# Performance work log

Hardware: AMD Instinct MI355X
Metric: run time of the kernel (lower is better)

## Reference

```python
import jax, jax.numpy as jnp
import numpy as np

B, L, ENC, DEC, ATT = 256, 196, 2048, 512, 512

def setup_inputs() -> dict:
    key = jax.random.key(0)
    ks = jax.random.split(key, 8)
    s_enc = 1.0 / np.sqrt(ENC); s_dec = 1.0 / np.sqrt(DEC); s_att = 1.0 / np.sqrt(ATT)
    return {
        "encoder_out": jax.random.normal(ks[0], (B, L, ENC), dtype=jnp.float32),
        "decoder_hidden": jax.random.normal(ks[1], (B, DEC), dtype=jnp.float32),
        "W_enc": jax.random.uniform(ks[2], (ENC, ATT), jnp.float32, -s_enc, s_enc),
        "b_enc": jax.random.uniform(ks[3], (ATT,), jnp.float32, -s_enc, s_enc),
        "W_dec": jax.random.uniform(ks[4], (DEC, ATT), jnp.float32, -s_dec, s_dec),
        "b_dec": jax.random.uniform(ks[5], (ATT,), jnp.float32, -s_dec, s_dec),
        "W_att": jax.random.uniform(ks[6], (ATT, 1), jnp.float32, -s_att, s_att),
        "b_att": jax.random.uniform(ks[7], (1,), jnp.float32, -s_att, s_att),
    }

def reference(encoder_out, decoder_hidden, W_enc, b_enc, W_dec, b_dec, W_att, b_att):
    # encoder_att: [B, L, A]; decoder_att: [B, A]
    encoder_att = jnp.einsum('ble,ea->bla', encoder_out, W_enc) + b_enc
    decoder_att = decoder_hidden @ W_dec + b_dec
    hidden = jax.nn.relu(encoder_att + decoder_att[:, None, :])  # [B, L, A]
    att = jnp.einsum('bla,a->bl', hidden, W_att[:, 0]) + b_att[0]  # [B, L]
    alpha = jax.nn.softmax(att, axis=1)  # softmax over sequence dim
    awe = jnp.einsum('ble,bl->be', encoder_out, alpha)  # weighted sum
    return awe, alpha
```

## Files before the change

kernel.cpp:

```cpp
#include <hip/hip_runtime.h>
#include <hip/hip_bf16.h>
#include <stdint.h>

#define NB 256
#define NL 196
#define NE 2048
#define ND 512
#define NA 512
#define NM (NB * NL)

typedef __attribute__((ext_vector_type(4))) float f32x4;
typedef __attribute__((ext_vector_type(8))) short bf16x8;

static __device__ __forceinline__ unsigned short f2bf(float f) {
  union { float f; uint32_t u; } c; c.f = f;
  uint32_t u = c.u;
  return (unsigned short)((u + 0x7fffu + ((u >> 16) & 1u)) >> 16);
}

__global__ void k_pack_b(const float* __restrict__ W, unsigned short* __restrict__ Bp) {
  int t = blockIdx.x * 256 + threadIdx.x;
  int lane = t & 63;
  int kt32 = (t >> 6) & 63;
  int ntile = t >> 12;
  int col = ntile * 16 + (lane & 15);
  int k0 = kt32 * 32 + ((lane >> 4) << 3);
  bf16x8 o;
#pragma unroll
  for (int j = 0; j < 8; ++j) o[j] = (short)f2bf(W[(size_t)(k0 + j) * NA + col]);
  *reinterpret_cast<bf16x8*>(Bp + ((size_t)t << 3)) = o;
}

__global__ void k_dec(const float* __restrict__ dec, const float* __restrict__ Wd,
                      const float* __restrict__ bd, const float* __restrict__ be,
                      float* __restrict__ d2) {
  __shared__ float dh[ND];
  int b = blockIdx.x, tid = threadIdx.x;
  dh[tid] = dec[(size_t)b * ND + tid];
  __syncthreads();
  float s = bd[tid] + be[tid];
#pragma unroll 8
  for (int e = 0; e < ND; ++e) s = fmaf(dh[e], Wd[(size_t)e * NA + tid], s);
  d2[(size_t)b * NA + tid] = s;
}

#define BM 64
#define BK 64
#define KT (NE / BK)

__global__ __launch_bounds__(512, 4) void k_main(
    const float* __restrict__ A,
    const unsigned short* __restrict__ Bp,
    const float* __restrict__ d2,
    const float* __restrict__ Watt,
    const float* __restrict__ batt,
    float* __restrict__ att)
{
  __shared__ unsigned short As[2][BM * BK];
  __shared__ float att_w[8][BM];

  const int tid = threadIdx.x;
  const int lane = tid & 63;
  const int wid = tid >> 6;
  const int lq = lane >> 4;
  const int lr = lane & 15;
  const int row0 = blockIdx.x * BM;

  f32x4 acc[4][4];
#pragma unroll
  for (int mf = 0; mf < 4; ++mf)
#pragma unroll
    for (int r = 0; r < 4; ++r) {
      int rowg = row0 + mf * 16 + lq * 4 + r;
      int bb = rowg / NL;
      const float* d2r = d2 + (size_t)bb * NA + wid * 64 + lr;
#pragma unroll
      for (int nf = 0; nf < 4; ++nf) acc[mf][nf][r] = d2r[nf * 16];
    }

  const int srow = tid >> 3;
  const int skc = tid & 7;
  const float* ag = A + (size_t)(row0 + srow) * NE + skc * 8;
  const int swz_w = srow * 64 + ((skc ^ (srow & 7)) << 3);

  auto cvt_store = [&](int buf, const f32x4& a, const f32x4& b) {
    bf16x8 o;
    o[0] = (short)f2bf(a[0]); o[1] = (short)f2bf(a[1]);
    o[2] = (short)f2bf(a[2]); o[3] = (short)f2bf(a[3]);
    o[4] = (short)f2bf(b[0]); o[5] = (short)f2bf(b[1]);
    o[6] = (short)f2bf(b[2]); o[7] = (short)f2bf(b[3]);
    *reinterpret_cast<bf16x8*>(&As[buf][swz_w]) = o;
  };

  {
    f32x4 p0 = *reinterpret_cast<const f32x4*>(ag);
    f32x4 p1 = *reinterpret_cast<const f32x4*>(ag + 4);
    cvt_store(0, p0, p1);
  }
  __syncthreads();

  const unsigned short* bpw = Bp + (size_t)(wid * 4) * 32768 + lane * 8;

  for (int kt = 0; kt < KT; ++kt) {
    const int cur = kt & 1;
    f32x4 n0, n1;
    if (kt < KT - 1) {
      const float* agn = ag + (size_t)(kt + 1) * BK;
      n0 = *reinterpret_cast<const f32x4*>(agn);
      n1 = *reinterpret_cast<const f32x4*>(agn + 4);
    }
    bf16x8 bf[4][2];
#pragma unroll
    for (int nf = 0; nf < 4; ++nf)
#pragma unroll
      for (int ks = 0; ks < 2; ++ks)
        bf[nf][ks] = *reinterpret_cast<const bf16x8*>(bpw + (size_t)nf * 32768 + (kt * 2 + ks) * 512);
#pragma unroll
    for (int ks = 0; ks < 2; ++ks)
#pragma unroll
      for (int mf = 0; mf < 4; ++mf) {
        const int rrow = mf * 16 + lr;
        const int chunk = (ks * 4 + lq) ^ (lr & 7);
        bf16x8 af = *reinterpret_cast<const bf16x8*>(&As[cur][rrow * 64 + (chunk << 3)]);
#pragma unroll
        for (int nf = 0; nf < 4; ++nf)
          acc[mf][nf] = __builtin_amdgcn_mfma_f32_16x16x32_bf16(af, bf[nf][ks], acc[mf][nf], 0, 0, 0);
      }
    if (kt < KT - 1) cvt_store(cur ^ 1, n0, n1);
    __syncthreads();
  }

  float w[4];
#pragma unroll
  for (int nf = 0; nf < 4; ++nf) w[nf] = Watt[wid * 64 + nf * 16 + lr];
#pragma unroll
  for (int mf = 0; mf < 4; ++mf)
#pragma unroll
    for (int r = 0; r < 4; ++r) {
      float s = 0.f;
#pragma unroll
      for (int nf = 0; nf < 4; ++nf) s = fmaf(fmaxf(acc[mf][nf][r], 0.f), w[nf], s);
      s += __shfl_xor(s, 1);
      s += __shfl_xor(s, 2);
      s += __shfl_xor(s, 4);
      s += __shfl_xor(s, 8);
      if (lr == 0) att_w[wid][mf * 16 + lq * 4 + r] = s;
    }
  __syncthreads();
  if (tid < BM) {
    float s = 0.f;
#pragma unroll
    for (int wv = 0; wv < 8; ++wv) s += att_w[wv][tid];
    att[row0 + tid] = s + batt[0];
  }
}

__global__ void k_softmax(float* __restrict__ alpha) {
  int b = blockIdx.x, lane = threadIdx.x;
  float* ar = alpha + (size_t)b * NL;
  float v[4];
#pragma unroll
  for (int i = 0; i < 4; ++i) {
    int l = i * 64 + lane;
    v[i] = (l < NL) ? ar[l] : -1e30f;
  }
  float m = fmaxf(fmaxf(v[0], v[1]), fmaxf(v[2], v[3]));
#pragma unroll
  for (int o = 32; o >= 1; o >>= 1) m = fmaxf(m, __shfl_xor(m, o));
  float e[4];
  float s = 0.f;
#pragma unroll
  for (int i = 0; i < 4; ++i) {
    int l = i * 64 + lane;
    e[i] = (l < NL) ? __expf(v[i] - m) : 0.f;
    s += e[i];
  }
#pragma unroll
  for (int o = 32; o >= 1; o >>= 1) s += __shfl_xor(s, o);
  float inv = 1.f / s;
#pragma unroll
  for (int i = 0; i < 4; ++i) {
    int l = i * 64 + lane;
    if (l < NL) ar[l] = e[i] * inv;
  }
}

__global__ void k_awe(const float* __restrict__ enc, const float* __restrict__ alpha,
                      float* __restrict__ awe) {
  __shared__ float al[NL];
  int b = blockIdx.y, ch = blockIdx.x, tid = threadIdx.x;
  if (tid < NL) al[tid] = alpha[(size_t)b * NL + tid];
  __syncthreads();
  int e0 = ch * 1024 + tid * 4;
  const float* ep = enc + (size_t)b * NL * NE + e0;
  f32x4 s = {0.f, 0.f, 0.f, 0.f};
#pragma unroll 4
  for (int l = 0; l < NL; ++l) {
    f32x4 v = *reinterpret_cast<const f32x4*>(ep + (size_t)l * NE);
    float a = al[l];
    s[0] = fmaf(a, v[0], s[0]);
    s[1] = fmaf(a, v[1], s[1]);
    s[2] = fmaf(a, v[2], s[2]);
    s[3] = fmaf(a, v[3], s[3]);
  }
  *reinterpret_cast<f32x4*>(awe + (size_t)b * NE + e0) = s;
}

extern "C" void kernel_launch(void* const* d_in, const int* in_sizes, int n_in,
                              void* d_out, int out_size, void* d_ws, size_t ws_size,
                              hipStream_t stream) {
  const float* enc  = (const float*)d_in[0];
  const float* dec  = (const float*)d_in[1];
  const float* Wenc = (const float*)d_in[2];
  const float* benc = (const float*)d_in[3];
  const float* Wdec = (const float*)d_in[4];
  const float* bdec = (const float*)d_in[5];
  const float* Watt = (const float*)d_in[6];
  const float* batt = (const float*)d_in[7];

  float* awe   = (float*)d_out;
  float* alpha = (float*)d_out + (size_t)NB * NE;

  char* ws = (char*)d_ws;
  unsigned short* Bp = (unsigned short*)ws;
  float* d2 = (float*)(ws + (size_t)2 * 1024 * 1024);

  k_pack_b<<<dim3(512), dim3(256), 0, stream>>>(Wenc, Bp);
  k_dec<<<dim3(NB), dim3(512), 0, stream>>>(dec, Wdec, bdec, benc, d2);
  k_main<<<dim3(NM / BM), dim3(512), 0, stream>>>(enc, Bp, d2, Watt, batt, alpha);
  k_softmax<<<dim3(NB), dim3(64), 0, stream>>>(alpha);
  k_awe<<<dim3(2, NB), dim3(256), 0, stream>>>(enc, alpha, awe);
}
```

Before: 264.5 us.

## Merge prep kernels and fuse softmax into weighted-sum kernel

New measurement: 256.8 us. 1.03x faster.

```diff
diff --git a/kernel.cpp b/kernel.cpp
--- a/kernel.cpp
+++ b/kernel.cpp
@@ -13,35 +13,38 @@
 typedef __attribute__((ext_vector_type(8))) short bf16x8;
 
 static __device__ __forceinline__ unsigned short f2bf(float f) {
-  union { float f; uint32_t u; } c; c.f = f;
-  uint32_t u = c.u;
-  return (unsigned short)((u + 0x7fffu + ((u >> 16) & 1u)) >> 16);
-}
-
-__global__ void k_pack_b(const float* __restrict__ W, unsigned short* __restrict__ Bp) {
-  int t = blockIdx.x * 256 + threadIdx.x;
-  int lane = t & 63;
-  int kt32 = (t >> 6) & 63;
-  int ntile = t >> 12;
-  int col = ntile * 16 + (lane & 15);
-  int k0 = kt32 * 32 + ((lane >> 4) << 3);
-  bf16x8 o;
-#pragma unroll
-  for (int j = 0; j < 8; ++j) o[j] = (short)f2bf(W[(size_t)(k0 + j) * NA + col]);
-  *reinterpret_cast<bf16x8*>(Bp + ((size_t)t << 3)) = o;
-}
-
-__global__ void k_dec(const float* __restrict__ dec, const float* __restrict__ Wd,
-                      const float* __restrict__ bd, const float* __restrict__ be,
-                      float* __restrict__ d2) {
-  __shared__ float dh[ND];
-  int b = blockIdx.x, tid = threadIdx.x;
-  dh[tid] = dec[(size_t)b * ND + tid];
-  __syncthreads();
-  float s = bd[tid] + be[tid];
+  __hip_bfloat16 h = __float2bfloat16(f);
+  unsigned short u;
+  __builtin_memcpy(&u, &h, 2);
+  return u;
+}
+
+__global__ __launch_bounds__(512) void k_prep(
+    const float* __restrict__ W, unsigned short* __restrict__ Bp,
+    const float* __restrict__ dec, const float* __restrict__ Wd,
+    const float* __restrict__ bd, const float* __restrict__ be,
+    float* __restrict__ d2) {
+  if (blockIdx.x < 256) {
+    int t = blockIdx.x * 512 + threadIdx.x;
+    int lane = t & 63;
+    int kt32 = (t >> 6) & 63;
+    int ntile = t >> 12;
+    int col = ntile * 16 + (lane & 15);
+    int k0 = kt32 * 32 + ((lane >> 4) << 3);
+    bf16x8 o;
+#pragma unroll
+    for (int j = 0; j < 8; ++j) o[j] = (short)f2bf(W[(size_t)(k0 + j) * NA + col]);
+    *reinterpret_cast<bf16x8*>(Bp + ((size_t)t << 3)) = o;
+  } else {
+    __shared__ float dh[ND];
+    int b = blockIdx.x - 256, tid = threadIdx.x;
+    dh[tid] = dec[(size_t)b * ND + tid];
+    __syncthreads();
+    float s = bd[tid] + be[tid];
 #pragma unroll 8
-  for (int e = 0; e < ND; ++e) s = fmaf(dh[e], Wd[(size_t)e * NA + tid], s);
-  d2[(size_t)b * NA + tid] = s;
+    for (int e = 0; e < ND; ++e) s = fmaf(dh[e], Wd[(size_t)e * NA + tid], s);
+    d2[(size_t)b * NA + tid] = s;
+  }
 }
 
 #define BM 64
@@ -155,55 +158,68 @@
   }
 }
 
-__global__ void k_softmax(float* __restrict__ alpha) {
-  int b = blockIdx.x, lane = threadIdx.x;
-  float* ar = alpha + (size_t)b * NL;
-  float v[4];
-#pragma unroll
-  for (int i = 0; i < 4; ++i) {
-    int l = i * 64 + lane;
-    v[i] = (l < NL) ? ar[l] : -1e30f;
-  }
-  float m = fmaxf(fmaxf(v[0], v[1]), fmaxf(v[2], v[3]));
-#pragma unroll
-  for (int o = 32; o >= 1; o >>= 1) m = fmaxf(m, __shfl_xor(m, o));
-  float e[4];
-  float s = 0.f;
-#pragma unroll
-  for (int i = 0; i < 4; ++i) {
-    int l = i * 64 + lane;
-    e[i] = (l < NL) ? __expf(v[i] - m) : 0.f;
-    s += e[i];
-  }
-#pragma unroll
-  for (int o = 32; o >= 1; o >>= 1) s += __shfl_xor(s, o);
-  float inv = 1.f / s;
-#pragma unroll
-  for (int i = 0; i < 4; ++i) {
-    int l = i * 64 + lane;
-    if (l < NL) ar[l] = e[i] * inv;
-  }
-}
-
-__global__ void k_awe(const float* __restrict__ enc, const float* __restrict__ alpha,
-                      float* __restrict__ awe) {
-  __shared__ float al[NL];
-  int b = blockIdx.y, ch = blockIdx.x, tid = threadIdx.x;
-  if (tid < NL) al[tid] = alpha[(size_t)b * NL + tid];
+__global__ __launch_bounds__(512) void k_awe(
+    const float* __restrict__ enc, const float* __restrict__ att,
+    float* __restrict__ alpha_out, float* __restrict__ awe) {
+  __shared__ float al[256];
+  const int b = blockIdx.x, tid = threadIdx.x;
+
+  if (tid < 64) {
+    const int lane = tid;
+    const float* ar = att + (size_t)b * NL;
+    float v[4];
+#pragma unroll
+    for (int i = 0; i < 4; ++i) {
+      int l = i * 64 + lane;
+      v[i] = (l < NL) ? ar[l] : -1e30f;
+    }
+    float m = fmaxf(fmaxf(v[0], v[1]), fmaxf(v[2], v[3]));
+#pragma unroll
+    for (int o = 32; o >= 1; o >>= 1) m = fmaxf(m, __shfl_xor(m, o));
+    float e[4];
+    float s = 0.f;
+#pragma unroll
+    for (int i = 0; i < 4; ++i) {
+      int l = i * 64 + lane;
+      e[i] = (l < NL) ? __expf(v[i] - m) : 0.f;
+      s += e[i];
+    }
+#pragma unroll
+    for (int o = 32; o >= 1; o >>= 1) s += __shfl_xor(s, o);
+    float inv = 1.f / s;
+#pragma unroll
+    for (int i = 0; i < 4; ++i) {
+      int l = i * 64 + lane;
+      if (l < NL) {
+        float a = e[i] * inv;
+        al[l] = a;
+        alpha_out[(size_t)b * NL + l] = a;
+      }
+    }
+  }
   __syncthreads();
-  int e0 = ch * 1024 + tid * 4;
-  const float* ep = enc + (size_t)b * NL * NE + e0;
-  f32x4 s = {0.f, 0.f, 0.f, 0.f};
-#pragma unroll 4
-  for (int l = 0; l < NL; ++l) {
-    f32x4 v = *reinterpret_cast<const f32x4*>(ep + (size_t)l * NE);
-    float a = al[l];
-    s[0] = fmaf(a, v[0], s[0]);
-    s[1] = fmaf(a, v[1], s[1]);
-    s[2] = fmaf(a, v[2], s[2]);
-    s[3] = fmaf(a, v[3], s[3]);
-  }
-  *reinterpret_cast<f32x4*>(awe + (size_t)b * NE + e0) = s;
+
+  const float* ep = enc + (size_t)b * NL * NE + tid * 4;
+  f32x4 a0 = {0.f, 0.f, 0.f, 0.f}, a1 = a0, a2 = a0, a3 = a0;
+#pragma unroll 2
+  for (int l = 0; l < NL; l += 4) {
+    f32x4 v0 = *reinterpret_cast<const f32x4*>(ep + (size_t)l * NE);
+    f32x4 v1 = *reinterpret_cast<const f32x4*>(ep + (size_t)(l + 1) * NE);
+    f32x4 v2 = *reinterpret_cast<const f32x4*>(ep + (size_t)(l + 2) * NE);
+    f32x4 v3 = *reinterpret_cast<const f32x4*>(ep + (size_t)(l + 3) * NE);
+    float c0 = al[l], c1 = al[l + 1], c2 = al[l + 2], c3 = al[l + 3];
+#pragma unroll
+    for (int j = 0; j < 4; ++j) {
+      a0[j] = fmaf(c0, v0[j], a0[j]);
+      a1[j] = fmaf(c1, v1[j], a1[j]);
+      a2[j] = fmaf(c2, v2[j], a2[j]);
+      a3[j] = fmaf(c3, v3[j], a3[j]);
+    }
+  }
+  f32x4 s4;
+#pragma unroll
+  for (int j = 0; j < 4; ++j) s4[j] = (a0[j] + a1[j]) + (a2[j] + a3[j]);
+  *reinterpret_cast<f32x4*>(awe + (size_t)b * NE + tid * 4) = s4;
 }
 
 extern "C" void kernel_launch(void* const* d_in, const int* in_sizes, int n_in,
@@ -223,11 +239,10 @@
 
   char* ws = (char*)d_ws;
   unsigned short* Bp = (unsigned short*)ws;
-  float* d2 = (float*)(ws + (size_t)2 * 1024 * 1024);
-
-  k_pack_b<<<dim3(512), dim3(256), 0, stream>>>(Wenc, Bp);
-  k_dec<<<dim3(NB), dim3(512), 0, stream>>>(dec, Wdec, bdec, benc, d2);
-  k_main<<<dim3(NM / BM), dim3(512), 0, stream>>>(enc, Bp, d2, Watt, batt, alpha);
-  k_softmax<<<dim3(NB), dim3(64), 0, stream>>>(alpha);
-  k_awe<<<dim3(2, NB), dim3(256), 0, stream>>>(enc, alpha, awe);
-}
+  float* d2  = (float*)(ws + (size_t)2 * 1024 * 1024);
+  float* att = (float*)(ws + (size_t)2 * 1024 * 1024 + 512 * 1024);
+
+  k_prep<<<dim3(512), dim3(512), 0, stream>>>(Wenc, Bp, dec, Wdec, bdec, benc, d2);
+  k_main<<<dim3(NM / BM), dim3(512), 0, stream>>>(enc, Bp, d2, Watt, batt, att);
+  k_awe<<<dim3(NB), dim3(512), 0, stream>>>(enc, att, alpha, awe);
+}
```
